# Performance work log

Hardware: AMD Instinct MI355X
Metric: run time of the kernel (lower is better)

The kernel has to match this reference:

```python
import jax, jax.numpy as jnp
import numpy as np

B, S, E, H = 8, 1024, 1024, 16
D = E // H          # head_dim = 64
FF = 4 * E          # mlp hidden = 4096
EPS = 1e-5


def setup_inputs() -> dict:
    key = jax.random.key(0)
    ks = jax.random.split(key, 12)
    s_e = 1.0 / np.sqrt(E)
    s_ff = 1.0 / np.sqrt(FF)
    return {
        "x": jax.random.normal(ks[0], (B, S, E), jnp.float32),
        # per-head q/k/v projections stacked: [H, E, D] (math layout: y = x @ W + b)
        "Wq": jax.random.normal(ks[1], (H, E, D), jnp.float32) * s_e,
        "bq": jnp.zeros((H, D), jnp.float32),
        "Wk": jax.random.normal(ks[2], (H, E, D), jnp.float32) * s_e,
        "bk": jnp.zeros((H, D), jnp.float32),
        "Wv": jax.random.normal(ks[3], (H, E, D), jnp.float32) * s_e,
        "bv": jnp.zeros((H, D), jnp.float32),
        # output projection [E, E]
        "Wo": jax.random.normal(ks[4], (E, E), jnp.float32) * s_e,
        "bo": jnp.zeros((E,), jnp.float32),
        # layernorms
        "g1": jnp.ones((E,), jnp.float32),
        "beta1": jnp.zeros((E,), jnp.float32),
        "g2": jnp.ones((E,), jnp.float32),
        "beta2": jnp.zeros((E,), jnp.float32),
        # MLP
        "W1": jax.random.normal(ks[5], (E, FF), jnp.float32) * s_e,
        "c1": jnp.zeros((FF,), jnp.float32),
        "W2": jax.random.normal(ks[6], (FF, E), jnp.float32) * s_ff,
        "c2": jnp.zeros((E,), jnp.float32),
    }


def _layernorm(x, g, b):
    mu = jnp.mean(x, axis=-1, keepdims=True)
    var = jnp.mean(jnp.square(x - mu), axis=-1, keepdims=True)
    return (x - mu) * jax.lax.rsqrt(var + EPS) * g + b


def _block(x, Wq, bq, Wk, bk, Wv, bv, Wo, bo, g1, beta1, g2, beta2, W1, c1, W2, c2):
    # --- attention sublayer (pre-norm) ---
    xn = _layernorm(x, g1, beta1)
    # all heads at once (equivalent to the per-head Python loop)
    q = jnp.einsum("bse,hed->bhsd", xn, Wq) + bq[:, None, :]
    k = jnp.einsum("bse,hed->bhsd", xn, Wk) + bk[:, None, :]
    v = jnp.einsum("bse,hed->bhsd", xn, Wv) + bv[:, None, :]
    scale = D ** -0.5
    scores = jnp.einsum("bhsd,bhtd->bhst", q, k) * scale  # [B,H,S,S]
    w = jax.nn.softmax(scores, axis=-1)
    ctx = jnp.einsum("bhst,bhtd->bhsd", w, v)             # [B,H,S,D]
    ctx = ctx.transpose(0, 2, 1, 3).reshape(x.shape[0], x.shape[1], E)  # concat heads
    attn_out = ctx @ Wo + bo
    x = x + attn_out
    # --- MLP sublayer (pre-norm) ---
    xn = _layernorm(x, g2, beta2)
    h = jax.nn.gelu(xn @ W1 + c1, approximate=False)
    return x + (h @ W2 + c2)


def reference(x, Wq, bq, Wk, bk, Wv, bv, Wo, bo, g1, beta1, g2, beta2, W1, c1, W2, c2):
    return _block(x, Wq, bq, Wk, bk, Wv, bv, Wo, bo, g1, beta1, g2, beta2, W1, c1, W2, c2)
```

## Files before the change

kernel.cpp:

```cpp
#include <hip/hip_runtime.h>
#include <math.h>


typedef _Float16 h16;
typedef __attribute__((ext_vector_type(8))) _Float16 f16x8;
typedef __attribute__((ext_vector_type(4))) float f32x4;

__device__ __forceinline__ void gl2lds16(const void* g, void* l) {
  __builtin_amdgcn_global_load_lds(
      (const __attribute__((address_space(1))) void*)g,
      (__attribute__((address_space(3))) void*)l, 16, 0, 0);
}

__global__ __launch_bounds__(256) void repack_kernel(
    const float* __restrict__ Wq, const float* __restrict__ Wk,
    const float* __restrict__ Wv, const float* __restrict__ Wo,
    const float* __restrict__ W1, const float* __restrict__ W2,
    const float* __restrict__ bq, const float* __restrict__ bk,
    const float* __restrict__ bv,
    h16* __restrict__ WqkvT, h16* __restrict__ WoT, h16* __restrict__ W1T,
    h16* __restrict__ W2T, float* __restrict__ bqkv)
{
  const int t = blockIdx.x;
  const int tid = threadIdx.x;
  if (t == 3072) {
    for (int i = tid; i < 3072; i += 256)
      bqkv[i] = (i < 1024) ? bq[i] : (i < 2048 ? bk[i - 1024] : bv[i - 2048]);
    return;
  }
  __shared__ float ld[64 * 65];

  const float* src; h16* dst;
  int sRS, dRS, k0, sn0, dn0;
  if (t < 768) {
    const int m = t >> 8, tt = t & 255, h = tt >> 4, tk = tt & 15;
    src = ((m == 0) ? Wq : (m == 1) ? Wk : Wv) + (size_t)h * 65536;
    dst = WqkvT; sRS = 64; dRS = 1024;
    k0 = tk * 64; sn0 = 0; dn0 = m * 1024 + h * 64;
  } else if (t < 1024) {
    const int tt = t - 768, tk = tt >> 4, tn = tt & 15;
    src = Wo; dst = WoT; sRS = 1024; dRS = 1024;
    k0 = tk * 64; sn0 = tn * 64; dn0 = tn * 64;
  } else if (t < 2048) {
    const int tt = t - 1024, tk = tt >> 6, tn = tt & 63;
    src = W1; dst = W1T; sRS = 4096; dRS = 1024;
    k0 = tk * 64; sn0 = tn * 64; dn0 = tn * 64;
  } else {
    const int tt = t - 2048, tk = tt >> 4, tn = tt & 15;
    src = W2; dst = W2T; sRS = 1024; dRS = 4096;
    k0 = tk * 64; sn0 = tn * 64; dn0 = tn * 64;
  }

  #pragma unroll
  for (int p = 0; p < 16; ++p) {
    const int idx = p * 256 + tid;
    const int r = idx >> 6, c = idx & 63;
    ld[c * 65 + r] = src[(size_t)(k0 + r) * sRS + sn0 + c];
  }
  __syncthreads();
  #pragma unroll
  for (int p = 0; p < 8; ++p) {
    const int idx = p * 512 + tid * 2;
    const int n = idx >> 6, k = idx & 63;
    union { unsigned int u; h16 e[2]; } pk;
    pk.e[0] = (h16)ld[n * 65 + k];
    pk.e[1] = (h16)ld[n * 65 + k + 1];
    *(unsigned int*)&dst[(size_t)(dn0 + n) * dRS + k0 + k] = pk.u;
  }
}

template <int IT>
__global__ __launch_bounds__(256) void ln_kernel(
    const void* __restrict__ in, const float* __restrict__ gw,
    const float* __restrict__ bw, h16* __restrict__ outp)
{
  const int row = blockIdx.x;
  const int tid = threadIdx.x;
  float v[4];
  if (IT == 0) {
    const float* p = (const float*)in + (size_t)row * 1024 + tid * 4;
    float4 tt = *(const float4*)p;
    v[0] = tt.x; v[1] = tt.y; v[2] = tt.z; v[3] = tt.w;
  } else {
    const h16* p = (const h16*)in + (size_t)row * 1024 + tid * 4;
    union { uint2 u; h16 h[4]; } raw;
    raw.u = *(const uint2*)p;
    v[0] = (float)raw.h[0]; v[1] = (float)raw.h[1];
    v[2] = (float)raw.h[2]; v[3] = (float)raw.h[3];
  }
  float s = v[0] + v[1] + v[2] + v[3];
  float ss = v[0]*v[0] + v[1]*v[1] + v[2]*v[2] + v[3]*v[3];
  #pragma unroll
  for (int off = 32; off >= 1; off >>= 1) {
    s += __shfl_down(s, off);
    ss += __shfl_down(ss, off);
  }
  __shared__ float red[8];
  const int w = tid >> 6;
  if ((tid & 63) == 0) { red[w] = s; red[4 + w] = ss; }
  __syncthreads();
  s = red[0] + red[1] + red[2] + red[3];
  ss = red[4] + red[5] + red[6] + red[7];
  const float mean = s * (1.0f / 1024.0f);
  const float var = ss * (1.0f / 1024.0f) - mean * mean;
  const float inv = rsqrtf(fmaxf(var, 0.0f) + 1e-5f);
  union { uint2 u; h16 h[4]; } pk;
  #pragma unroll
  for (int i = 0; i < 4; ++i)
    pk.h[i] = (h16)((v[i] - mean) * inv * gw[tid * 4 + i] + bw[tid * 4 + i]);
  *(uint2*)(outp + (size_t)row * 1024 + tid * 4) = pk.u;
}

#define GEMM_LDS 147456

template <int MODE>
__global__ __launch_bounds__(512, 2) void gemm_bt(
    const h16* __restrict__ A, const h16* __restrict__ BT,
    const float* __restrict__ bias, const void* __restrict__ res,
    void* __restrict__ out, int M, int N, int K)
{
  extern __shared__ __align__(16) char smem[];
  const int tid = threadIdx.x;
  const int lane = tid & 63, w = tid >> 6;
  const int l15 = lane & 15, quad = lane >> 4;
  const int wm = w >> 1, wn = w & 1;
  const int m0 = blockIdx.y * 256, n0 = blockIdx.x * 128;
  const int NT = K >> 6;

  const int srow = w * 8 + (lane >> 3);
  const int scol = ((lane & 7) ^ ((lane >> 3) & 7)) * 8;
  const h16* gA = A + (size_t)(m0 + srow) * K + scol;
  const h16* gB = BT + (size_t)(n0 + srow) * K + scol;
  const int ldsw = w * 1024;

  const int arow = wm * 64 + l15;
  const int brow = wn * 64 + l15;
  const int x7 = l15 & 7;
  const int sw0 = (quad ^ x7) << 4;
  const int sw1 = ((4 | quad) ^ x7) << 4;

  f32x4 zero = {0.f, 0.f, 0.f, 0.f};
  f32x4 acc[4][4];
  #pragma unroll
  for (int a = 0; a < 4; ++a)
    #pragma unroll
    for (int b = 0; b < 4; ++b) acc[a][b] = zero;

  {
    char* b0 = smem;
    char* b1 = smem + 49152;
    #pragma unroll
    for (int j = 0; j < 4; ++j) gl2lds16(gA + (size_t)j * 64 * K, b0 + j * 8192 + ldsw);
    #pragma unroll
    for (int j = 0; j < 2; ++j) gl2lds16(gB + (size_t)j * 64 * K, b0 + 32768 + j * 8192 + ldsw);
    #pragma unroll
    for (int j = 0; j < 4; ++j) gl2lds16(gA + 64 + (size_t)j * 64 * K, b1 + j * 8192 + ldsw);
    #pragma unroll
    for (int j = 0; j < 2; ++j) gl2lds16(gB + 64 + (size_t)j * 64 * K, b1 + 32768 + j * 8192 + ldsw);
  }
  asm volatile("s_waitcnt vmcnt(6)" ::: "memory");
  __builtin_amdgcn_sched_barrier(0);
  __builtin_amdgcn_s_barrier();

  int cur = 0, pre = 2;
  for (int t = 0; t < NT; ++t) {
    const char* Ab = smem + cur * 49152;
    const char* Bb = Ab + 32768;
    char* Pb = smem + pre * 49152;
    const bool pf = (t + 2) < NT;
    f16x8 af[4][2], bf[4][2];

    #pragma unroll
    for (int mi = 0; mi < 4; ++mi) {
      af[mi][0] = *(const f16x8*)(Ab + (arow + mi * 16) * 128 + sw0);
      af[mi][1] = *(const f16x8*)(Ab + (arow + mi * 16) * 128 + sw1);
    }
    #pragma unroll
    for (int ni = 0; ni < 2; ++ni) {
      bf[ni][0] = *(const f16x8*)(Bb + (brow + ni * 16) * 128 + sw0);
      bf[ni][1] = *(const f16x8*)(Bb + (brow + ni * 16) * 128 + sw1);
    }
    if (pf) {
      const h16* g = gA + (size_t)(t + 2) * 64;
      #pragma unroll
      for (int j = 0; j < 4; ++j) gl2lds16(g + (size_t)j * 64 * K, Pb + j * 8192 + ldsw);
    }
    __builtin_amdgcn_s_barrier();
    __builtin_amdgcn_s_setprio(1);
    #pragma unroll
    for (int mi = 0; mi < 4; ++mi)
      #pragma unroll
      for (int ni = 0; ni < 2; ++ni) {
        acc[mi][ni] = __builtin_amdgcn_mfma_f32_16x16x32_f16(af[mi][0], bf[ni][0], acc[mi][ni], 0, 0, 0);
        acc[mi][ni] = __builtin_amdgcn_mfma_f32_16x16x32_f16(af[mi][1], bf[ni][1], acc[mi][ni], 0, 0, 0);
      }
    __builtin_amdgcn_s_setprio(0);
    __builtin_amdgcn_s_barrier();

    #pragma unroll
    for (int ni = 2; ni < 4; ++ni) {
      bf[ni][0] = *(const f16x8*)(Bb + (brow + ni * 16) * 128 + sw0);
      bf[ni][1] = *(const f16x8*)(Bb + (brow + ni * 16) * 128 + sw1);
    }
    if (pf) {
      const h16* g = gB + (size_t)(t + 2) * 64;
      #pragma unroll
      for (int j = 0; j < 2; ++j) gl2lds16(g + (size_t)j * 64 * K, Pb + 32768 + j * 8192 + ldsw);
    }
    __builtin_amdgcn_s_barrier();
    __builtin_amdgcn_s_setprio(1);
    #pragma unroll
    for (int mi = 0; mi < 4; ++mi)
      #pragma unroll
      for (int ni = 2; ni < 4; ++ni) {
        acc[mi][ni] = __builtin_amdgcn_mfma_f32_16x16x32_f16(af[mi][0], bf[ni][0], acc[mi][ni], 0, 0, 0);
        acc[mi][ni] = __builtin_amdgcn_mfma_f32_16x16x32_f16(af[mi][1], bf[ni][1], acc[mi][ni], 0, 0, 0);
      }
    __builtin_amdgcn_s_setprio(0);
    if (pf) {
      asm volatile("s_waitcnt vmcnt(6)" ::: "memory");
    } else if (t + 2 == NT) {
      asm volatile("s_waitcnt vmcnt(0)" ::: "memory");
    }
    __builtin_amdgcn_sched_barrier(0);
    __builtin_amdgcn_s_barrier();
    cur = (cur == 2) ? 0 : cur + 1;
    pre = (pre == 2) ? 0 : pre + 1;
  }

  #pragma unroll
  for (int mi = 0; mi < 4; ++mi) {
    #pragma unroll
    for (int ni = 0; ni < 4; ++ni) {
      #pragma unroll
      for (int i = 0; i < 4; ++i) {
        const int r = m0 + wm * 64 + mi * 16 + quad * 4 + i;
        const int c = n0 + wn * 64 + ni * 16 + l15;
        const size_t idx = (size_t)r * N + c;
        float v = acc[mi][ni][i] + bias[c];
        if (MODE == 0) {
          ((h16*)out)[idx] = (h16)v;
        } else if (MODE == 1) {
          v += ((const float*)res)[idx];
          ((h16*)out)[idx] = (h16)v;
        } else if (MODE == 2) {
          const float e = __expf(v * (-1.5957691216f - 0.0713548163f * v * v));
          v = v / (1.0f + e);
          ((h16*)out)[idx] = (h16)v;
        } else {
          v += (float)((const h16*)res)[idx];
          ((float*)out)[idx] = v;
        }
      }
    }
  }
}

__global__ __launch_bounds__(256, 2) void attn_kernel(
    const h16* __restrict__ qkv, h16* __restrict__ ctx)
{
  const int qb = blockIdx.x;
  const int bh = blockIdx.y;
  const int b = bh >> 4, h = bh & 15;
  const int tid = threadIdx.x;
  const int w = tid >> 6, lane = tid & 63;
  const int l15 = lane & 15, quad = lane >> 4;

  __shared__ __align__(16) h16 Ks[64 * 80];
  __shared__ __align__(16) h16 Vt[64 * 80];
  __shared__ __align__(16) h16 Ps[256 * 80];

  const size_t qrow0 = (size_t)(b * 1024 + qb * 256);
  for (int c = tid; c < 2048; c += 256) {
    const int row = c >> 3, kc = (c & 7) * 8;
    uint4 raw = *(const uint4*)(qkv + (qrow0 + row) * 3072 + h * 64 + kc);
    union { uint4 v; h16 e[8]; } in4, out4;
    in4.v = raw;
    #pragma unroll
    for (int i = 0; i < 8; ++i) out4.e[i] = in4.e[i] * (h16)0.125f;
    *(uint4*)&Ps[row * 80 + kc] = out4.v;
  }
  __syncthreads();
  f16x8 aq[4][2];
  #pragma unroll
  for (int r = 0; r < 4; ++r)
    #pragma unroll
    for (int s = 0; s < 2; ++s)
      aq[r][s] = *(const f16x8*)&Ps[(w * 64 + r * 16 + l15) * 80 + s * 32 + quad * 8];

  f32x4 zero = {0.f, 0.f, 0.f, 0.f};
  f32x4 o_acc[4][4];
  float l_p[4][4];
  #pragma unroll
  for (int r = 0; r < 4; ++r)
    #pragma unroll
    for (int i = 0; i < 4; ++i) { o_acc[r][i] = zero; l_p[r][i] = 0.f; }

  h16* Pw = &Ps[w * 64 * 80];

  for (int jt = 0; jt < 16; ++jt) {
    __syncthreads();
    const size_t kv0 = (size_t)(b * 1024 + jt * 64);
    for (int c = tid; c < 512; c += 256) {
      const int row = c >> 3, kc = (c & 7) * 8;
      *(uint4*)&Ks[row * 80 + kc] =
          *(const uint4*)(qkv + (kv0 + row) * 3072 + 1024 + h * 64 + kc);
    }
    #pragma unroll
    for (int cc = 0; cc < 2; ++cc) {
      const int d0 = (w + cc * 4) * 8;
      uint4 raw = *(const uint4*)(qkv + (kv0 + lane) * 3072 + 2048 + h * 64 + d0);
      union { uint4 v; h16 e[8]; } in4;
      in4.v = raw;
      #pragma unroll
      for (int i = 0; i < 8; ++i) Vt[(d0 + i) * 80 + lane] = in4.e[i];
    }
    __syncthreads();

    f16x8 kf[4][2];
    #pragma unroll
    for (int ni = 0; ni < 4; ++ni)
      #pragma unroll
      for (int s = 0; s < 2; ++s)
        kf[ni][s] = *(const f16x8*)&Ks[(ni * 16 + l15) * 80 + s * 32 + quad * 8];
    #pragma unroll
    for (int r = 0; r < 4; ++r) {
      f32x4 s_acc[4];
      #pragma unroll
      for (int i = 0; i < 4; ++i) s_acc[i] = zero;
      #pragma unroll
      for (int ni = 0; ni < 4; ++ni)
        #pragma unroll
        for (int s = 0; s < 2; ++s)
          s_acc[ni] = __builtin_amdgcn_mfma_f32_16x16x32_f16(aq[r][s], kf[ni][s], s_acc[ni], 0, 0, 0);
      #pragma unroll
      for (int ni = 0; ni < 4; ++ni)
        #pragma unroll
        for (int i = 0; i < 4; ++i) {
          float p = __expf(s_acc[ni][i]);
          l_p[r][i] += p;
          Pw[(r * 16 + quad * 4 + i) * 80 + ni * 16 + l15] = (h16)p;
        }
    }

    f16x8 vf[4][2];
    #pragma unroll
    for (int ni = 0; ni < 4; ++ni)
      #pragma unroll
      for (int s = 0; s < 2; ++s)
        vf[ni][s] = *(const f16x8*)&Vt[(ni * 16 + l15) * 80 + s * 32 + quad * 8];
    #pragma unroll
    for (int r = 0; r < 4; ++r) {
      f16x8 ap0 = *(const f16x8*)&Pw[(r * 16 + l15) * 80 + quad * 8];
      f16x8 ap1 = *(const f16x8*)&Pw[(r * 16 + l15) * 80 + 32 + quad * 8];
      #pragma unroll
      for (int ni = 0; ni < 4; ++ni) {
        o_acc[r][ni] = __builtin_amdgcn_mfma_f32_16x16x32_f16(ap0, vf[ni][0], o_acc[r][ni], 0, 0, 0);
        o_acc[r][ni] = __builtin_amdgcn_mfma_f32_16x16x32_f16(ap1, vf[ni][1], o_acc[r][ni], 0, 0, 0);
      }
    }
  }

  #pragma unroll
  for (int r = 0; r < 4; ++r)
    #pragma unroll
    for (int i = 0; i < 4; ++i) {
      float lt = l_p[r][i];
      #pragma unroll
      for (int off = 1; off < 16; off <<= 1) lt += __shfl_xor(lt, off);
      const float rinv = 1.0f / lt;
      const size_t row = qrow0 + w * 64 + r * 16 + quad * 4 + i;
      #pragma unroll
      for (int ni = 0; ni < 4; ++ni)
        ctx[row * 1024 + h * 64 + ni * 16 + l15] = (h16)(o_acc[r][ni][i] * rinv);
    }
}

extern "C" void kernel_launch(void* const* d_in, const int* in_sizes, int n_in,
                              void* d_out, int out_size, void* d_ws, size_t ws_size,
                              hipStream_t stream) {
  const float* x   = (const float*)d_in[0];
  const float* Wq  = (const float*)d_in[1];
  const float* bq  = (const float*)d_in[2];
  const float* Wk  = (const float*)d_in[3];
  const float* bk  = (const float*)d_in[4];
  const float* Wv  = (const float*)d_in[5];
  const float* bv  = (const float*)d_in[6];
  const float* Wo  = (const float*)d_in[7];
  const float* bo  = (const float*)d_in[8];
  const float* g1  = (const float*)d_in[9];
  const float* be1 = (const float*)d_in[10];
  const float* g2  = (const float*)d_in[11];
  const float* be2 = (const float*)d_in[12];
  const float* W1  = (const float*)d_in[13];
  const float* c1  = (const float*)d_in[14];
  const float* W2  = (const float*)d_in[15];
  const float* c2  = (const float*)d_in[16];

  char* ws = (char*)d_ws;
  h16*   WqkvT = (h16*)(ws + 0);
  h16*   WoT   = (h16*)(ws + 6291456);
  h16*   W1T   = (h16*)(ws + 8388608);
  h16*   W2T   = (h16*)(ws + 16777216);
  float* bqkv  = (float*)(ws + 25165824);
  h16*   bufA  = (h16*)(ws + 25178112);
  h16*   qkv   = (h16*)(ws + 41955328);
  h16*   x1    = (h16*)(ws + 41955328);
  h16*   hbuf  = (h16*)(ws + 58732544);

  static bool attr_done = false;
  if (!attr_done) {
    hipFuncSetAttribute((const void*)gemm_bt<0>, hipFuncAttributeMaxDynamicSharedMemorySize, GEMM_LDS);
    hipFuncSetAttribute((const void*)gemm_bt<1>, hipFuncAttributeMaxDynamicSharedMemorySize, GEMM_LDS);
    hipFuncSetAttribute((const void*)gemm_bt<2>, hipFuncAttributeMaxDynamicSharedMemorySize, GEMM_LDS);
    hipFuncSetAttribute((const void*)gemm_bt<3>, hipFuncAttributeMaxDynamicSharedMemorySize, GEMM_LDS);
    attr_done = true;
  }

  repack_kernel<<<dim3(3073), dim3(256), 0, stream>>>(Wq, Wk, Wv, Wo, W1, W2, bq, bk, bv,
                                                      WqkvT, WoT, W1T, W2T, bqkv);
  ln_kernel<0><<<dim3(8192), dim3(256), 0, stream>>>(x, g1, be1, bufA);
  gemm_bt<0><<<dim3(24, 32), dim3(512), GEMM_LDS, stream>>>(bufA, WqkvT, bqkv, nullptr, qkv,
                                                            8192, 3072, 1024);
  attn_kernel<<<dim3(4, 128), dim3(256), 0, stream>>>(qkv, bufA);
  gemm_bt<1><<<dim3(8, 32), dim3(512), GEMM_LDS, stream>>>(bufA, WoT, bo, x, x1,
                                                           8192, 1024, 1024);
  ln_kernel<1><<<dim3(8192), dim3(256), 0, stream>>>(x1, g2, be2, bufA);
  gemm_bt<2><<<dim3(32, 32), dim3(512), GEMM_LDS, stream>>>(bufA, W1T, c1, nullptr, hbuf,
                                                            8192, 4096, 1024);
  gemm_bt<3><<<dim3(8, 32), dim3(512), GEMM_LDS, stream>>>(hbuf, W2T, c2, x1, d_out,
                                                           8192, 1024, 4096);
}
```

Measured before the change: 511.6 us.

## Add 256x256-tile GEMM with 4-stage K=32 pipeline for QKV and MLP-up projections

Introduces a new GEMM kernel using 256x256 output tiles, 8 waves in a 2x4 arrangement, K-step 32 and a 4-buffer LDS ring with prefetch three tiles ahead. It replaces the 256x128 GEMM for the QKV and W1 projections, raising arithmetic intensity per block and halving the grid. The per-wave accumulator grows to 8x4 MFMA tiles, which raises register pressure and may hurt occupancy. The existing GEMM also splits its A-fragment loads into two separate arrays to change the load ordering.

```diff
diff --git a/kernel.cpp b/kernel.cpp
--- a/kernel.cpp
+++ b/kernel.cpp
@@ -111,6 +111,133 @@
   *(uint2*)(outp + (size_t)row * 1024 + tid * 4) = pk.u;
 }
 
+#define GEMM8_LDS 131072
+
+template <int MODE>
+__global__ __launch_bounds__(512, 2) void gemm8_bt(
+    const h16* __restrict__ A, const h16* __restrict__ BT,
+    const float* __restrict__ bias, const void* __restrict__ res,
+    void* __restrict__ out, int M, int N, int K)
+{
+  extern __shared__ __align__(16) char smem[];
+  const int tid = threadIdx.x;
+  const int lane = tid & 63;
+  const int l15 = lane & 15, quad = lane >> 4;
+  const int w = tid >> 6;
+  const int wr = w >> 2, wc = w & 3;
+  const int m0 = blockIdx.y * 256, n0 = blockIdx.x * 256;
+  const int NT = K >> 5;
+
+  const int sk = (((tid & 3) ^ ((tid >> 3) & 3)) << 3);
+  const h16* gA = A + (size_t)(m0 + (tid >> 2)) * K + sk;
+  const h16* gB = BT + (size_t)(n0 + (tid >> 2)) * K + sk;
+  const int d0 = tid * 16;
+
+  const int x4 = (quad ^ ((l15 >> 1) & 3)) << 4;
+  const int aoff = (wr * 128 + l15) * 64 + x4;
+  const int boff = 16384 + (wc * 64 + l15) * 64 + x4;
+
+  f32x4 zero = {0.f, 0.f, 0.f, 0.f};
+  f32x4 acc[8][4];
+  #pragma unroll
+  for (int a = 0; a < 8; ++a)
+    #pragma unroll
+    for (int b = 0; b < 4; ++b) acc[a][b] = zero;
+
+  #pragma unroll
+  for (int tt = 0; tt < 3; ++tt) {
+    char* bp = smem + tt * 32768;
+    gl2lds16(gA + (size_t)tt * 32, bp + d0);
+    gl2lds16(gA + (size_t)tt * 32 + (size_t)128 * K, bp + 8192 + d0);
+    gl2lds16(gB + (size_t)tt * 32, bp + 16384 + d0);
+    gl2lds16(gB + (size_t)tt * 32 + (size_t)128 * K, bp + 24576 + d0);
+  }
+  asm volatile("s_waitcnt vmcnt(8)" ::: "memory");
+  __builtin_amdgcn_sched_barrier(0);
+  __builtin_amdgcn_s_barrier();
+
+  for (int t = 0; t < NT; ++t) {
+    const char* Tb = smem + (t & 3) * 32768;
+    char* Pb = smem + ((t + 3) & 3) * 32768;
+    const bool pf = (t + 3) < NT;
+    f16x8 bf[4], af[4], af2[4];
+
+    #pragma unroll
+    for (int ni = 0; ni < 4; ++ni)
+      bf[ni] = *(const f16x8*)(Tb + boff + ni * 1024);
+    #pragma unroll
+    for (int mi = 0; mi < 4; ++mi)
+      af[mi] = *(const f16x8*)(Tb + aoff + mi * 1024);
+    if (pf) {
+      const h16* g = gA + (size_t)(t + 3) * 32;
+      gl2lds16(g, Pb + d0);
+      gl2lds16(g + (size_t)128 * K, Pb + 8192 + d0);
+    }
+    __builtin_amdgcn_s_barrier();
+    __builtin_amdgcn_s_setprio(1);
+    #pragma unroll
+    for (int mi = 0; mi < 4; ++mi)
+      #pragma unroll
+      for (int ni = 0; ni < 4; ++ni)
+        acc[mi][ni] = __builtin_amdgcn_mfma_f32_16x16x32_f16(af[mi], bf[ni], acc[mi][ni], 0, 0, 0);
+    __builtin_amdgcn_s_setprio(0);
+
+    #pragma unroll
+    for (int mi = 0; mi < 4; ++mi)
+      af2[mi] = *(const f16x8*)(Tb + aoff + (mi + 4) * 1024);
+    if (pf) {
+      const h16* g = gB + (size_t)(t + 3) * 32;
+      gl2lds16(g, Pb + 16384 + d0);
+      gl2lds16(g + (size_t)128 * K, Pb + 24576 + d0);
+    }
+    __builtin_amdgcn_s_barrier();
+    __builtin_amdgcn_s_setprio(1);
+    #pragma unroll
+    for (int mi = 0; mi < 4; ++mi)
+      #pragma unroll
+      for (int ni = 0; ni < 4; ++ni)
+        acc[mi + 4][ni] = __builtin_amdgcn_mfma_f32_16x16x32_f16(af2[mi], bf[ni], acc[mi + 4][ni], 0, 0, 0);
+    __builtin_amdgcn_s_setprio(0);
+
+    if (pf) {
+      asm volatile("s_waitcnt vmcnt(8)" ::: "memory");
+    } else if (t + 3 == NT) {
+      asm volatile("s_waitcnt vmcnt(4)" ::: "memory");
+    } else if (t + 2 == NT) {
+      asm volatile("s_waitcnt vmcnt(0)" ::: "memory");
+    }
+    __builtin_amdgcn_sched_barrier(0);
+    __builtin_amdgcn_s_barrier();
+  }
+
+  #pragma unroll
+  for (int mi = 0; mi < 8; ++mi) {
+    #pragma unroll
+    for (int ni = 0; ni < 4; ++ni) {
+      #pragma unroll
+      for (int i = 0; i < 4; ++i) {
+        const int r = m0 + wr * 128 + mi * 16 + quad * 4 + i;
+        const int c = n0 + wc * 64 + ni * 16 + l15;
+        const size_t idx = (size_t)r * N + c;
+        float v = acc[mi][ni][i] + bias[c];
+        if (MODE == 0) {
+          ((h16*)out)[idx] = (h16)v;
+        } else if (MODE == 1) {
+          v += ((const float*)res)[idx];
+          ((h16*)out)[idx] = (h16)v;
+        } else if (MODE == 2) {
+          const float e = __expf(v * (-1.5957691216f - 0.0713548163f * v * v));
+          v = v / (1.0f + e);
+          ((h16*)out)[idx] = (h16)v;
+        } else {
+          v += (float)((const h16*)res)[idx];
+          ((float*)out)[idx] = v;
+        }
+      }
+    }
+  }
+}
+
 #define GEMM_LDS 147456
 
 template <int MODE>
@@ -168,13 +295,16 @@
     const char* Bb = Ab + 32768;
     char* Pb = smem + pre * 49152;
     const bool pf = (t + 2) < NT;
-    f16x8 af[4][2], bf[4][2];
+    f16x8 af[4], bf[4][2];
 
     #pragma unroll
     for (int mi = 0; mi < 4; ++mi) {
-      af[mi][0] = *(const f16x8*)(Ab + (arow + mi * 16) * 128 + sw0);
-      af[mi][1] = *(const f16x8*)(Ab + (arow + mi * 16) * 128 + sw1);
-    }
+      af[mi] = *(const f16x8*)(Ab + (arow + mi * 16) * 128 + sw0);
+    }
+    f16x8 af1[4];
+    #pragma unroll
+    for (int mi = 0; mi < 4; ++mi)
+      af1[mi] = *(const f16x8*)(Ab + (arow + mi * 16) * 128 + sw1);
     #pragma unroll
     for (int ni = 0; ni < 2; ++ni) {
       bf[ni][0] = *(const f16x8*)(Bb + (brow + ni * 16) * 128 + sw0);
@@ -191,8 +321,8 @@
     for (int mi = 0; mi < 4; ++mi)
       #pragma unroll
       for (int ni = 0; ni < 2; ++ni) {
-        acc[mi][ni] = __builtin_amdgcn_mfma_f32_16x16x32_f16(af[mi][0], bf[ni][0], acc[mi][ni], 0, 0, 0);
-        acc[mi][ni] = __builtin_amdgcn_mfma_f32_16x16x32_f16(af[mi][1], bf[ni][1], acc[mi][ni], 0, 0, 0);
+        acc[mi][ni] = __builtin_amdgcn_mfma_f32_16x16x32_f16(af[mi], bf[ni][0], acc[mi][ni], 0, 0, 0);
+        acc[mi][ni] = __builtin_amdgcn_mfma_f32_16x16x32_f16(af1[mi], bf[ni][1], acc[mi][ni], 0, 0, 0);
       }
     __builtin_amdgcn_s_setprio(0);
     __builtin_amdgcn_s_barrier();
@@ -213,8 +343,8 @@
     for (int mi = 0; mi < 4; ++mi)
       #pragma unroll
       for (int ni = 2; ni < 4; ++ni) {
-        acc[mi][ni] = __builtin_amdgcn_mfma_f32_16x16x32_f16(af[mi][0], bf[ni][0], acc[mi][ni], 0, 0, 0);
-        acc[mi][ni] = __builtin_amdgcn_mfma_f32_16x16x32_f16(af[mi][1], bf[ni][1], acc[mi][ni], 0, 0, 0);
+        acc[mi][ni] = __builtin_amdgcn_mfma_f32_16x16x32_f16(af[mi], bf[ni][0], acc[mi][ni], 0, 0, 0);
+        acc[mi][ni] = __builtin_amdgcn_mfma_f32_16x16x32_f16(af1[mi], bf[ni][1], acc[mi][ni], 0, 0, 0);
       }
     __builtin_amdgcn_s_setprio(0);
     if (pf) {
@@ -410,24 +540,24 @@
 
   static bool attr_done = false;
   if (!attr_done) {
-    hipFuncSetAttribute((const void*)gemm_bt<0>, hipFuncAttributeMaxDynamicSharedMemorySize, GEMM_LDS);
     hipFuncSetAttribute((const void*)gemm_bt<1>, hipFuncAttributeMaxDynamicSharedMemorySize, GEMM_LDS);
-    hipFuncSetAttribute((const void*)gemm_bt<2>, hipFuncAttributeMaxDynamicSharedMemorySize, GEMM_LDS);
     hipFuncSetAttribute((const void*)gemm_bt<3>, hipFuncAttributeMaxDynamicSharedMemorySize, GEMM_LDS);
+    hipFuncSetAttribute((const void*)gemm8_bt<0>, hipFuncAttributeMaxDynamicSharedMemorySize, GEMM8_LDS);
+    hipFuncSetAttribute((const void*)gemm8_bt<2>, hipFuncAttributeMaxDynamicSharedMemorySize, GEMM8_LDS);
     attr_done = true;
   }
 
   repack_kernel<<<dim3(3073), dim3(256), 0, stream>>>(Wq, Wk, Wv, Wo, W1, W2, bq, bk, bv,
                                                       WqkvT, WoT, W1T, W2T, bqkv);
   ln_kernel<0><<<dim3(8192), dim3(256), 0, stream>>>(x, g1, be1, bufA);
-  gemm_bt<0><<<dim3(24, 32), dim3(512), GEMM_LDS, stream>>>(bufA, WqkvT, bqkv, nullptr, qkv,
-                                                            8192, 3072, 1024);
+  gemm8_bt<0><<<dim3(12, 32), dim3(512), GEMM8_LDS, stream>>>(bufA, WqkvT, bqkv, nullptr, qkv,
+                                                              8192, 3072, 1024);
   attn_kernel<<<dim3(4, 128), dim3(256), 0, stream>>>(qkv, bufA);
   gemm_bt<1><<<dim3(8, 32), dim3(512), GEMM_LDS, stream>>>(bufA, WoT, bo, x, x1,
                                                            8192, 1024, 1024);
   ln_kernel<1><<<dim3(8192), dim3(256), 0, stream>>>(x1, g2, be2, bufA);
-  gemm_bt<2><<<dim3(32, 32), dim3(512), GEMM_LDS, stream>>>(bufA, W1T, c1, nullptr, hbuf,
-                                                            8192, 4096, 1024);
+  gemm8_bt<2><<<dim3(16, 32), dim3(512), GEMM8_LDS, stream>>>(bufA, W1T, c1, nullptr, hbuf,
+                                                              8192, 4096, 1024);
   gemm_bt<3><<<dim3(8, 32), dim3(512), GEMM_LDS, stream>>>(hbuf, W2T, c2, x1, d_out,
                                                            8192, 1024, 4096);
 }
```

Measured after the change: 506.8 us. No clear change (-0.9%).
